# Kernel tuning notes

Measured on AMD Instinct MI355X. Metric: run time of the kernel, lower is better.

The kernel has to match this reference:

```python
import jax, jax.numpy as jnp
import numpy as np

EPS = 1e-08


def setup_inputs() -> dict:
    key = jax.random.key(0)
    k1, k2, k3 = jax.random.split(key, 3)
    B, T, IN, OUT = 32, 500, 2048, 1024
    x = jax.random.normal(k1, (B, T, IN), dtype=jnp.float32)
    # torch init: normal(mean=0, std=w_init_std*sqrt(1/input_shape))
    w = jax.random.normal(k2, (IN, OUT), dtype=jnp.float32) * np.sqrt(1.0 / IN)
    # b ~ N(1.0, 0.01), clamped >= 0
    b = jnp.clip(1.0 + 0.01 * jax.random.normal(k3, (OUT,), dtype=jnp.float32), 0.0, None)
    decay_m = jnp.array([0.6], dtype=jnp.float32)  # N(0.6, .01) clamped to [0,1]
    decay_s = jnp.array([0.9], dtype=jnp.float32)  # N(0.9, .01) clamped to [0,1]
    return {"x": x, "w": w, "b": b, "decay_m": decay_m, "decay_s": decay_s}


def reference(x, w, b, decay_m, decay_s):
    # x: [B, T, IN]; w: [IN, OUT]
    B, T, _ = x.shape
    OUT = w.shape[1]
    h = jnp.einsum('btc,cd->btd', x, w)          # [B, T, OUT]
    norm = jnp.sum(w * w, axis=0)                 # [OUT]
    dm = decay_m[0]
    ds = decay_s[0]
    inv_norm = 1.0 / (norm + EPS)
    zeros = jnp.zeros((B, OUT), dtype=x.dtype)
    # spk is never assigned a spike value in the original forward (spike_fn
    # is never applied), so it remains zero throughout.
    spk = zeros

    def step(carry, inp):
        M, S, E = carry
        E = dm * norm * (E + spk)                 # spk == 0 (faithful to source)
        M = dm * (M + inp)
        S = ds * (S + inp)
        mem = M - S - E
        mthr = mem * inv_norm - b                 # [B, OUT]
        return (M, S, E), mthr

    (_, _, _), spk_rec_t = jax.lax.scan(step, (zeros, zeros, zeros),
                                        jnp.swapaxes(h, 0, 1))  # [T, B, OUT]
    spk_rec = jnp.swapaxes(spk_rec_t, 0, 1)       # [B, T, OUT]
    loss = 0.5 * jnp.mean(spk_rec ** 2)
    return (spk_rec, loss)
```

## Files before the change

kernel.cpp:

```cpp
#include <hip/hip_runtime.h>


typedef __bf16 bf16x8 __attribute__((ext_vector_type(8)));
typedef __bf16 bf16x4 __attribute__((ext_vector_type(4)));
typedef float  f32x4  __attribute__((ext_vector_type(4)));

#define BDIM 32
#define TDIM 500
#define INDIM 2048
#define OUTDIM 1024
#define MROWS 16000
#define NCHUNK 25
#define CHLEN 20
#define OUT_ELEMS 16384000

__device__ __forceinline__ void gld_lds16(const void* g, void* l) {
    __builtin_amdgcn_global_load_lds(
        (const __attribute__((address_space(1))) unsigned int*)g,
        (__attribute__((address_space(3))) unsigned int*)l, 16, 0, 0);
}

__global__ void convert_x(const float* __restrict__ x, __bf16* __restrict__ xb) {
    size_t i = ((size_t)blockIdx.x * 256 + threadIdx.x) * 8;
    float4 a = *(const float4*)(x + i);
    float4 b = *(const float4*)(x + i + 4);
    bf16x8 o;
    o[0] = (__bf16)a.x; o[1] = (__bf16)a.y; o[2] = (__bf16)a.z; o[3] = (__bf16)a.w;
    o[4] = (__bf16)b.x; o[5] = (__bf16)b.y; o[6] = (__bf16)b.z; o[7] = (__bf16)b.w;
    *(bf16x8*)(xb + i) = o;
}

__global__ void transpose_w(const float* __restrict__ w, __bf16* __restrict__ wbt,
                            float* __restrict__ normAcc) {
    __shared__ float tile[32][33];
    __shared__ float red[8][33];
    const int tx = threadIdx.x;
    const int ty = threadIdx.y;
    const int d0 = blockIdx.x * 32;
    const int c0 = blockIdx.y * 32;
    float s = 0.f;
#pragma unroll
    for (int i = 0; i < 4; ++i) {
        int c = c0 + ty + i * 8;
        float v = w[(size_t)c * OUTDIM + d0 + tx];
        tile[ty + i * 8][tx] = v;
        s += v * v;
    }
    red[ty][tx] = s;
    __syncthreads();
#pragma unroll
    for (int i = 0; i < 4; ++i) {
        int d = d0 + ty + i * 8;
        wbt[(size_t)d * INDIM + c0 + tx] = (__bf16)tile[tx][ty + i * 8];
    }
    if (ty == 0) {
        float t = red[0][tx] + red[1][tx] + red[2][tx] + red[3][tx]
                + red[4][tx] + red[5][tx] + red[6][tx] + red[7][tx];
        atomicAdd(&normAcc[d0 + tx], t);
    }
}

__global__ __launch_bounds__(512, 2) void gemm_bf16(
    const __bf16* __restrict__ A,
    const __bf16* __restrict__ Bt,
    __bf16* __restrict__ H)
{
    constexpr int K  = INDIM;
    constexpr int NT = K / 32;
    __shared__ __align__(16) __bf16 As[4][256 * 32];
    __shared__ __align__(16) __bf16 Bs[4][256 * 32];

    const int tid  = threadIdx.x;
    const int wave = tid >> 6;
    const int lane = tid & 63;
    const int wm   = wave >> 2;
    const int wn   = wave & 3;

    const int orig = blockIdx.x;
    const int xcd = orig & 7, within = orig >> 3;
    const int wgid = (xcd < 4) ? (xcd * 32 + within)
                               : (128 + (xcd - 4) * 31 + within);
    const int bm = (wgid >> 2) * 256;
    const int bn = (wgid & 3) * 256;

    const int srow = lane >> 2;
    const int sseg = lane & 3;
    const int scol = (sseg ^ ((srow >> 1) & 3)) * 8;
    const int lds0 = (wave * 16) * 32;
    const int lds1 = (128 + wave * 16) * 32;
    int rA0 = bm +       wave * 16 + srow; if (rA0 > MROWS - 1) rA0 = MROWS - 1;
    int rA1 = bm + 128 + wave * 16 + srow; if (rA1 > MROWS - 1) rA1 = MROWS - 1;
    const __bf16* gA0 = A  + (size_t)rA0 * K + scol;
    const __bf16* gA1 = A  + (size_t)rA1 * K + scol;
    const __bf16* gB0 = Bt + (size_t)(bn +       wave * 16 + srow) * K + scol;
    const __bf16* gB1 = Bt + (size_t)(bn + 128 + wave * 16 + srow) * K + scol;

    const int mrow = lane & 15, quad = lane >> 4;
    const int swzq = quad ^ ((mrow >> 1) & 3);
    const int rdA = (wm * 128 + mrow) * 32 + swzq * 8;
    const int rdB = (wn * 64  + mrow) * 32 + swzq * 8;

    f32x4 acc[8][4] = {};

#define STAGE(tt) do { const int _b = (tt) & 3; const size_t _k = (size_t)(tt) * 32; \
        gld_lds16(gA0 + _k, &As[_b][lds0]);                                          \
        gld_lds16(gA1 + _k, &As[_b][lds1]);                                          \
        gld_lds16(gB0 + _k, &Bs[_b][lds0]);                                          \
        gld_lds16(gB1 + _k, &Bs[_b][lds1]); } while (0)

    STAGE(0); STAGE(1); STAGE(2); STAGE(3);
    asm volatile("s_waitcnt vmcnt(12)" ::: "memory");
    asm volatile("s_barrier" ::: "memory");

#pragma unroll 1
    for (int t = 0; t < NT; ++t) {
        const __bf16* as = As[t & 3];
        const __bf16* bs = Bs[t & 3];
        bf16x8 af[8], bfr[4];
#pragma unroll
        for (int i = 0; i < 8; ++i) af[i]  = *(const bf16x8*)&as[rdA + i * 512];
#pragma unroll
        for (int j = 0; j < 4; ++j) bfr[j] = *(const bf16x8*)&bs[rdB + j * 512];
#pragma unroll
        for (int i = 0; i < 8; ++i)
#pragma unroll
            for (int j = 0; j < 4; ++j)
                acc[i][j] = __builtin_amdgcn_mfma_f32_16x16x32_bf16(
                    af[i], bfr[j], acc[i][j], 0, 0, 0);
        asm volatile("s_barrier" ::: "memory");
        if (t + 4 < NT) STAGE(t + 4);
        if (t < NT - 4)       asm volatile("s_waitcnt vmcnt(12)" ::: "memory");
        else if (t == NT - 4) asm volatile("s_waitcnt vmcnt(8)"  ::: "memory");
        else if (t == NT - 3) asm volatile("s_waitcnt vmcnt(4)"  ::: "memory");
        else if (t == NT - 2) asm volatile("s_waitcnt vmcnt(0)"  ::: "memory");
        if (t < NT - 1) asm volatile("s_barrier" ::: "memory");
    }
#undef STAGE

    const int Rb = bm + wm * 128 + quad * 4;
    const int Cb = bn + wn * 64 + mrow;
#pragma unroll
    for (int i = 0; i < 8; ++i)
#pragma unroll
        for (int j = 0; j < 4; ++j)
#pragma unroll
            for (int r = 0; r < 4; ++r) {
                const int R = Rb + i * 16 + r;
                if (R < MROWS)
                    H[(size_t)R * OUTDIM + Cb + j * 16] = (__bf16)acc[i][j][r];
            }
}

__global__ void scan1(const __bf16* __restrict__ H,
                      f32x4* __restrict__ cM, f32x4* __restrict__ cS,
                      const float* __restrict__ dmp, const float* __restrict__ dsp) {
    const float dm = *dmp, ds = *dsp;
    const int c = blockIdx.x, b = blockIdx.y, tid = threadIdx.x;
    f32x4 M = {}, S = {};
    const __bf16* p = H + ((size_t)b * TDIM + c * CHLEN) * OUTDIM + tid * 4;
#pragma unroll 4
    for (int t = 0; t < CHLEN; ++t) {
        bf16x4 hv = *(const bf16x4*)(p + (size_t)t * OUTDIM);
        f32x4 h; h[0] = hv[0]; h[1] = hv[1]; h[2] = hv[2]; h[3] = hv[3];
        M = dm * (M + h);
        S = ds * (S + h);
    }
    const size_t idx = ((size_t)c * BDIM + b) * 256 + tid;
    cM[idx] = M;
    cS[idx] = S;
}

__global__ void scan2(float* __restrict__ cM, float* __restrict__ cS,
                      const float* __restrict__ dmp, const float* __restrict__ dsp) {
    const float dm = *dmp, ds = *dsp;
    float km = 1.f, ks = 1.f;
#pragma unroll
    for (int i = 0; i < CHLEN; ++i) { km *= dm; ks *= ds; }
    const int gid = blockIdx.x * 256 + threadIdx.x;
    const int b = gid >> 10, d = gid & 1023;
    float tM = 0.f, tS = 0.f;
    for (int c = 0; c < NCHUNK; ++c) {
        const size_t idx = (((size_t)c * BDIM + b) << 10) + d;
        float oM = cM[idx], oS = cS[idx];
        cM[idx] = tM; cS[idx] = tS;
        tM = km * tM + oM;
        tS = ks * tS + oS;
    }
}

__global__ void scan3(const __bf16* __restrict__ H,
                      const f32x4* __restrict__ cM, const f32x4* __restrict__ cS,
                      const float* __restrict__ normAcc, const float* __restrict__ bias,
                      const float* __restrict__ dmp, const float* __restrict__ dsp,
                      float* __restrict__ out, float* __restrict__ lossAcc,
                      unsigned* __restrict__ ticket) {
    const float dm = *dmp, ds = *dsp;
    const int c = blockIdx.x, b = blockIdx.y, tid = threadIdx.x;
    const size_t cidx = ((size_t)c * BDIM + b) * 256 + tid;
    f32x4 M = cM[cidx];
    f32x4 S = cS[cidx];
    f32x4 nv = *(const f32x4*)(normAcc + tid * 4);
    f32x4 inv;
    inv[0] = 1.f / (nv[0] + 1e-8f); inv[1] = 1.f / (nv[1] + 1e-8f);
    inv[2] = 1.f / (nv[2] + 1e-8f); inv[3] = 1.f / (nv[3] + 1e-8f);
    f32x4 bv = *(const f32x4*)(bias + tid * 4);

    const size_t rowbase = ((size_t)b * TDIM + c * CHLEN) * OUTDIM + tid * 4;
    const __bf16* p = H + rowbase;
    float* o = out + rowbase;
    float loss = 0.f;
#pragma unroll 4
    for (int t = 0; t < CHLEN; ++t) {
        bf16x4 hv = *(const bf16x4*)(p + (size_t)t * OUTDIM);
        f32x4 h; h[0] = hv[0]; h[1] = hv[1]; h[2] = hv[2]; h[3] = hv[3];
        M = dm * (M + h);
        S = ds * (S + h);
        f32x4 r = (M - S) * inv - bv;
        *(f32x4*)(o + (size_t)t * OUTDIM) = r;
        loss += r[0] * r[0] + r[1] * r[1] + r[2] * r[2] + r[3] * r[3];
    }
    __shared__ float red[256];
    red[tid] = loss;
    __syncthreads();
    for (int s = 128; s > 0; s >>= 1) {
        if (tid < s) red[tid] += red[tid + s];
        __syncthreads();
    }
    if (tid == 0) {
        atomicAdd(lossAcc, red[0]);
        __threadfence();
        unsigned t = atomicAdd(ticket, 1u);
        if (t == NCHUNK * BDIM - 1) {
            float total = atomicAdd(lossAcc, 0.0f);
            out[OUT_ELEMS] = 0.5f * total / (float)OUT_ELEMS;
        }
    }
}

#define OFF_H      ((size_t)0)
#define OFF_WBT    ((size_t)32768000)
#define OFF_NORM   ((size_t)36962304)
#define OFF_LOSS   ((size_t)36966400)
#define OFF_TICKET ((size_t)36966404)
#define OFF_CM     ((size_t)36966656)
#define OFF_CS     ((size_t)40243456)

extern "C" void kernel_launch(void* const* d_in, const int* in_sizes, int n_in,
                              void* d_out, int out_size, void* d_ws, size_t ws_size,
                              hipStream_t stream) {
    const float* x  = (const float*)d_in[0];
    const float* w  = (const float*)d_in[1];
    const float* bb = (const float*)d_in[2];
    const float* dm = (const float*)d_in[3];
    const float* ds = (const float*)d_in[4];

    char* ws = (char*)d_ws;
    __bf16*   H    = (__bf16*)(ws + OFF_H);
    __bf16*   WBT  = (__bf16*)(ws + OFF_WBT);
    float*    NORM = (float*)(ws + OFF_NORM);
    float*    LOSS = (float*)(ws + OFF_LOSS);
    unsigned* TICK = (unsigned*)(ws + OFF_TICKET);
    f32x4*    CM   = (f32x4*)(ws + OFF_CM);
    f32x4*    CS   = (f32x4*)(ws + OFF_CS);
    __bf16*   XB   = (__bf16*)d_out;
    float*    out  = (float*)d_out;

    hipMemsetAsync(ws + OFF_NORM, 0, 4096 + 256, stream);

    convert_x<<<16000, 256, 0, stream>>>(x, XB);
    transpose_w<<<dim3(32, 64), dim3(32, 8), 0, stream>>>(w, WBT, NORM);
    gemm_bf16<<<252, 512, 0, stream>>>(XB, WBT, H);
    scan1<<<dim3(NCHUNK, BDIM), 256, 0, stream>>>(H, CM, CS, dm, ds);
    scan2<<<128, 256, 0, stream>>>((float*)CM, (float*)CS, dm, ds);
    scan3<<<dim3(NCHUNK, BDIM), 256, 0, stream>>>(H, CM, CS, NORM, bb, dm, ds,
                                                  out, LOSS, TICK);
}
```

Measured before the change: 347.3 us.

## Fuse fp32-to-bf16 conversion of x into GEMM A-tile loading

Drops the separate convert_x kernel. The GEMM now reads fp32 x directly through register prefetch two steps ahead, converts it to bf16, and writes it into swizzled LDS, while B stays on direct global-to-LDS loads. The k-step is split into two half-tiles of 4x4 MFMAs with finer-grained waits and barriers. This removes a full write and re-read of the bf16 copy of x. In exchange the GEMM reads twice as many A bytes, holds more registers, and runs conversion ALU work inside the main loop.

```diff
diff --git a/kernel.cpp b/kernel.cpp
--- a/kernel.cpp
+++ b/kernel.cpp
@@ -18,16 +18,6 @@
     __builtin_amdgcn_global_load_lds(
         (const __attribute__((address_space(1))) unsigned int*)g,
         (__attribute__((address_space(3))) unsigned int*)l, 16, 0, 0);
-}
-
-__global__ void convert_x(const float* __restrict__ x, __bf16* __restrict__ xb) {
-    size_t i = ((size_t)blockIdx.x * 256 + threadIdx.x) * 8;
-    float4 a = *(const float4*)(x + i);
-    float4 b = *(const float4*)(x + i + 4);
-    bf16x8 o;
-    o[0] = (__bf16)a.x; o[1] = (__bf16)a.y; o[2] = (__bf16)a.z; o[3] = (__bf16)a.w;
-    o[4] = (__bf16)b.x; o[5] = (__bf16)b.y; o[6] = (__bf16)b.z; o[7] = (__bf16)b.w;
-    *(bf16x8*)(xb + i) = o;
 }
 
 __global__ void transpose_w(const float* __restrict__ w, __bf16* __restrict__ wbt,
@@ -60,8 +50,8 @@
     }
 }
 
-__global__ __launch_bounds__(512, 2) void gemm_bf16(
-    const __bf16* __restrict__ A,
+__global__ __launch_bounds__(512, 2) void gemm_fused(
+    const float* __restrict__ A,
     const __bf16* __restrict__ Bt,
     __bf16* __restrict__ H)
 {
@@ -83,17 +73,21 @@
     const int bm = (wgid >> 2) * 256;
     const int bn = (wgid & 3) * 256;
 
+    const int rloc = tid >> 1;
+    const int asub = tid & 1;
+    int arow = bm + rloc; if (arow > MROWS - 1) arow = MROWS - 1;
+    const float* aSrc = A + (size_t)arow * K + asub * 16;
+    const int fA = (rloc >> 1) & 3;
+    const int wbOff0 = rloc * 32 + ((2 * asub)     ^ fA) * 8;
+    const int wbOff1 = rloc * 32 + ((2 * asub + 1) ^ fA) * 8;
+
     const int srow = lane >> 2;
     const int sseg = lane & 3;
     const int scol = (sseg ^ ((srow >> 1) & 3)) * 8;
-    const int lds0 = (wave * 16) * 32;
-    const int lds1 = (128 + wave * 16) * 32;
-    int rA0 = bm +       wave * 16 + srow; if (rA0 > MROWS - 1) rA0 = MROWS - 1;
-    int rA1 = bm + 128 + wave * 16 + srow; if (rA1 > MROWS - 1) rA1 = MROWS - 1;
-    const __bf16* gA0 = A  + (size_t)rA0 * K + scol;
-    const __bf16* gA1 = A  + (size_t)rA1 * K + scol;
-    const __bf16* gB0 = Bt + (size_t)(bn +       wave * 16 + srow) * K + scol;
-    const __bf16* gB1 = Bt + (size_t)(bn + 128 + wave * 16 + srow) * K + scol;
+    const __bf16* gB0 = Bt + (size_t)(bn + (wave * 2 + 0) * 16 + srow) * K + scol;
+    const __bf16* gB1 = Bt + (size_t)(bn + (wave * 2 + 1) * 16 + srow) * K + scol;
+    const int ldsB0 = (wave * 2 + 0) * 512;
+    const int ldsB1 = (wave * 2 + 1) * 512;
 
     const int mrow = lane & 15, quad = lane >> 4;
     const int swzq = quad ^ ((mrow >> 1) & 3);
@@ -101,41 +95,85 @@
     const int rdB = (wn * 64  + mrow) * 32 + swzq * 8;
 
     f32x4 acc[8][4] = {};
-
-#define STAGE(tt) do { const int _b = (tt) & 3; const size_t _k = (size_t)(tt) * 32; \
-        gld_lds16(gA0 + _k, &As[_b][lds0]);                                          \
-        gld_lds16(gA1 + _k, &As[_b][lds1]);                                          \
-        gld_lds16(gB0 + _k, &Bs[_b][lds0]);                                          \
-        gld_lds16(gB1 + _k, &Bs[_b][lds1]); } while (0)
-
-    STAGE(0); STAGE(1); STAGE(2); STAGE(3);
-    asm volatile("s_waitcnt vmcnt(12)" ::: "memory");
+    f32x4 gl0[4], gl1[4];
+
+#define ALOAD(G, TT) do { const float* s_ = aSrc + (size_t)(TT) * 32;           \
+        G[0] = *(const f32x4*)(s_);      G[1] = *(const f32x4*)(s_ + 4);        \
+        G[2] = *(const f32x4*)(s_ + 8);  G[3] = *(const f32x4*)(s_ + 12); } while (0)
+
+#define AWB(G, TT) do { __bf16* ad_ = &As[(TT) & 3][0]; bf16x8 o0_, o1_;        \
+        o0_[0]=(__bf16)G[0][0]; o0_[1]=(__bf16)G[0][1]; o0_[2]=(__bf16)G[0][2]; \
+        o0_[3]=(__bf16)G[0][3]; o0_[4]=(__bf16)G[1][0]; o0_[5]=(__bf16)G[1][1]; \
+        o0_[6]=(__bf16)G[1][2]; o0_[7]=(__bf16)G[1][3];                         \
+        o1_[0]=(__bf16)G[2][0]; o1_[1]=(__bf16)G[2][1]; o1_[2]=(__bf16)G[2][2]; \
+        o1_[3]=(__bf16)G[2][3]; o1_[4]=(__bf16)G[3][0]; o1_[5]=(__bf16)G[3][1]; \
+        o1_[6]=(__bf16)G[3][2]; o1_[7]=(__bf16)G[3][3];                         \
+        *(bf16x8*)(ad_ + wbOff0) = o0_; *(bf16x8*)(ad_ + wbOff1) = o1_; } while (0)
+
+#define BSTAGE(TT) do {                                                          \
+        gld_lds16(gB0 + (size_t)(TT) * 32, &Bs[(TT) & 3][ldsB0]);                \
+        gld_lds16(gB1 + (size_t)(TT) * 32, &Bs[(TT) & 3][ldsB1]); } while (0)
+
+    ALOAD(gl0, 0);
+    ALOAD(gl1, 1);
+    asm volatile("s_waitcnt vmcnt(4)" ::: "memory");
+    AWB(gl0, 0);
+    ALOAD(gl0, 2);
+    asm volatile("s_waitcnt vmcnt(4)" ::: "memory");
+    AWB(gl1, 1);
+    ALOAD(gl1, 3);
+    asm volatile("s_waitcnt vmcnt(4)" ::: "memory");
+    AWB(gl0, 2);
+    BSTAGE(0); BSTAGE(1); BSTAGE(2);
+    asm volatile("s_waitcnt vmcnt(4) lgkmcnt(0)" ::: "memory");
     asm volatile("s_barrier" ::: "memory");
 
+#define KSTEP(T, GI, GC) do {                                                    \
+        const __bf16* as_ = &As[(T) & 3][0];                                     \
+        const __bf16* bs_ = &Bs[(T) & 3][0];                                     \
+                        \
+        if ((T) + 4 < NT) ALOAD(GI, (T) + 4);                                    \
+        if ((T) <= NT - 5)      asm volatile("s_waitcnt vmcnt(6)" ::: "memory"); \
+        else if ((T) <= NT - 3) asm volatile("s_waitcnt vmcnt(2)" ::: "memory"); \
+        else if ((T) == NT - 2) asm volatile("s_waitcnt vmcnt(0)" ::: "memory"); \
+        if ((T) + 3 < NT) AWB(GC, (T) + 3);                                      \
+        bf16x8 a_[4], b_[4];                                                     \
+        _Pragma("unroll")                                                        \
+        for (int i = 0; i < 4; ++i) a_[i] = *(const bf16x8*)&as_[rdA + i * 512]; \
+        _Pragma("unroll")                                                        \
+        for (int j = 0; j < 4; ++j) b_[j] = *(const bf16x8*)&bs_[rdB + j * 512]; \
+        asm volatile("s_waitcnt lgkmcnt(0)" ::: "memory");                       \
+        _Pragma("unroll")                                                        \
+        for (int i = 0; i < 4; ++i)                                              \
+        _Pragma("unroll")                                                        \
+            for (int j = 0; j < 4; ++j)                                          \
+                acc[i][j] = __builtin_amdgcn_mfma_f32_16x16x32_bf16(             \
+                    a_[i], b_[j], acc[i][j], 0, 0, 0);                           \
+        asm volatile("s_barrier" ::: "memory");                                  \
+                                     \
+        if ((T) + 3 < NT) BSTAGE((T) + 3);                                       \
+        _Pragma("unroll")                                                        \
+        for (int i = 0; i < 4; ++i)                                              \
+            a_[i] = *(const bf16x8*)&as_[rdA + 2048 + i * 512];                  \
+        asm volatile("s_waitcnt lgkmcnt(0)" ::: "memory");                       \
+        _Pragma("unroll")                                                        \
+        for (int i = 0; i < 4; ++i)                                              \
+        _Pragma("unroll")                                                        \
+            for (int j = 0; j < 4; ++j)                                          \
+                acc[4 + i][j] = __builtin_amdgcn_mfma_f32_16x16x32_bf16(         \
+                    a_[i], b_[j], acc[4 + i][j], 0, 0, 0);                       \
+        asm volatile("s_barrier" ::: "memory");                                  \
+    } while (0)
+
 #pragma unroll 1
-    for (int t = 0; t < NT; ++t) {
-        const __bf16* as = As[t & 3];
-        const __bf16* bs = Bs[t & 3];
-        bf16x8 af[8], bfr[4];
-#pragma unroll
-        for (int i = 0; i < 8; ++i) af[i]  = *(const bf16x8*)&as[rdA + i * 512];
-#pragma unroll
-        for (int j = 0; j < 4; ++j) bfr[j] = *(const bf16x8*)&bs[rdB + j * 512];
-#pragma unroll
-        for (int i = 0; i < 8; ++i)
-#pragma unroll
-            for (int j = 0; j < 4; ++j)
-                acc[i][j] = __builtin_amdgcn_mfma_f32_16x16x32_bf16(
-                    af[i], bfr[j], acc[i][j], 0, 0, 0);
-        asm volatile("s_barrier" ::: "memory");
-        if (t + 4 < NT) STAGE(t + 4);
-        if (t < NT - 4)       asm volatile("s_waitcnt vmcnt(12)" ::: "memory");
-        else if (t == NT - 4) asm volatile("s_waitcnt vmcnt(8)"  ::: "memory");
-        else if (t == NT - 3) asm volatile("s_waitcnt vmcnt(4)"  ::: "memory");
-        else if (t == NT - 2) asm volatile("s_waitcnt vmcnt(0)"  ::: "memory");
-        if (t < NT - 1) asm volatile("s_barrier" ::: "memory");
-    }
-#undef STAGE
+    for (int t = 0; t < NT; t += 2) {
+        KSTEP(t,     gl0, gl1);
+        KSTEP(t + 1, gl1, gl0);
+    }
+#undef KSTEP
+#undef ALOAD
+#undef AWB
+#undef BSTAGE
 
     const int Rb = bm + wm * 128 + quad * 4;
     const int Cb = bn + wn * 64 + mrow;
@@ -262,14 +300,12 @@
     unsigned* TICK = (unsigned*)(ws + OFF_TICKET);
     f32x4*    CM   = (f32x4*)(ws + OFF_CM);
     f32x4*    CS   = (f32x4*)(ws + OFF_CS);
-    __bf16*   XB   = (__bf16*)d_out;
     float*    out  = (float*)d_out;
 
     hipMemsetAsync(ws + OFF_NORM, 0, 4096 + 256, stream);
 
-    convert_x<<<16000, 256, 0, stream>>>(x, XB);
     transpose_w<<<dim3(32, 64), dim3(32, 8), 0, stream>>>(w, WBT, NORM);
-    gemm_bf16<<<252, 512, 0, stream>>>(XB, WBT, H);
+    gemm_fused<<<252, 512, 0, stream>>>(x, WBT, H);
     scan1<<<dim3(NCHUNK, BDIM), 256, 0, stream>>>(H, CM, CS, dm, ds);
     scan2<<<128, 256, 0, stream>>>((float*)CM, (float*)CS, dm, ds);
     scan3<<<dim3(NCHUNK, BDIM), 256, 0, stream>>>(H, CM, CS, NORM, bb, dm, ds,
```

New measurement: 343.4 us. Within noise of the previous version (-1.1%).

## Restructure GEMM mainloop into quadrant-split double-buffered K64 pipeline with interleaved loads

Applied to the files above, without the earlier changes.

Rewrites the bf16 GEMM main loop to use K-steps of 64 with a two-buffer LDS scheme. Each 256x256 tile is split into quadrants (A halves × B halves), and global→LDS loads for the next tile are interleaved between the four MFMA quadrant phases, each phase guarded by its own barrier. It also raises MFMA wave priority around compute blocks, with the aim of hiding load latency and cutting LDS read pressure per MFMA. The cost is more barriers per iteration and a more fragile, hand-tuned vmcnt schedule.

```diff
diff --git a/kernel.cpp b/kernel.cpp
--- a/kernel.cpp
+++ b/kernel.cpp
@@ -66,9 +66,9 @@
     __bf16* __restrict__ H)
 {
     constexpr int K  = INDIM;
-    constexpr int NT = K / 32;
-    __shared__ __align__(16) __bf16 As[4][256 * 32];
-    __shared__ __align__(16) __bf16 Bs[4][256 * 32];
+    constexpr int NT = K / 64;
+    __shared__ __align__(16) __bf16 SA[2][2][2][4096];
+    __shared__ __align__(16) __bf16 SB[2][2][2][4096];
 
     const int tid  = threadIdx.x;
     const int wave = tid >> 6;
@@ -86,69 +86,108 @@
     const int srow = lane >> 2;
     const int sseg = lane & 3;
     const int scol = (sseg ^ ((srow >> 1) & 3)) * 8;
-    const int lds0 = (wave * 16) * 32;
-    const int lds1 = (128 + wave * 16) * 32;
-    int rA0 = bm +       wave * 16 + srow; if (rA0 > MROWS - 1) rA0 = MROWS - 1;
-    int rA1 = bm + 128 + wave * 16 + srow; if (rA1 > MROWS - 1) rA1 = MROWS - 1;
-    const __bf16* gA0 = A  + (size_t)rA0 * K + scol;
-    const __bf16* gA1 = A  + (size_t)rA1 * K + scol;
-    const __bf16* gB0 = Bt + (size_t)(bn +       wave * 16 + srow) * K + scol;
-    const __bf16* gB1 = Bt + (size_t)(bn + 128 + wave * 16 + srow) * K + scol;
+    int ra0 = bm +       wave * 16 + srow; if (ra0 > MROWS - 1) ra0 = MROWS - 1;
+    int ra1 = bm + 128 + wave * 16 + srow; if (ra1 > MROWS - 1) ra1 = MROWS - 1;
+    const __bf16* pA0 = A  + (size_t)ra0 * K + scol;
+    const __bf16* pA1 = A  + (size_t)ra1 * K + scol;
+    const __bf16* pB0 = Bt + (size_t)(bn +       wave * 16 + srow) * K + scol;
+    const __bf16* pB1 = Bt + (size_t)(bn + 128 + wave * 16 + srow) * K + scol;
+    const int sdst = wave * 512;
 
     const int mrow = lane & 15, quad = lane >> 4;
     const int swzq = quad ^ ((mrow >> 1) & 3);
-    const int rdA = (wm * 128 + mrow) * 32 + swzq * 8;
-    const int rdB = (wn * 64  + mrow) * 32 + swzq * 8;
+    const int rdA = (wm * 64 + mrow) * 32 + swzq * 8;
+    const int rdB = (wn * 32 + mrow) * 32 + swzq * 8;
 
     f32x4 acc[8][4] = {};
-
-#define STAGE(tt) do { const int _b = (tt) & 3; const size_t _k = (size_t)(tt) * 32; \
-        gld_lds16(gA0 + _k, &As[_b][lds0]);                                          \
-        gld_lds16(gA1 + _k, &As[_b][lds1]);                                          \
-        gld_lds16(gB0 + _k, &Bs[_b][lds0]);                                          \
-        gld_lds16(gB1 + _k, &Bs[_b][lds1]); } while (0)
-
-    STAGE(0); STAGE(1); STAGE(2); STAGE(3);
-    asm volatile("s_waitcnt vmcnt(12)" ::: "memory");
+    bf16x8 a[4][2], b[2][2];
+
+#define STG_A(NB, HH, T1) do { const __bf16* p_ = (HH) ? pA1 : pA0;            \
+        gld_lds16(p_ + (size_t)(T1) * 64,      &SA[NB][HH][0][sdst]);          \
+        gld_lds16(p_ + (size_t)(T1) * 64 + 32, &SA[NB][HH][1][sdst]); } while (0)
+#define STG_B(NB, HH, T1) do { const __bf16* p_ = (HH) ? pB1 : pB0;            \
+        gld_lds16(p_ + (size_t)(T1) * 64,      &SB[NB][HH][0][sdst]);          \
+        gld_lds16(p_ + (size_t)(T1) * 64 + 32, &SB[NB][HH][1][sdst]); } while (0)
+#define RD_A(BUF, HH) do { _Pragma("unroll")                                   \
+        for (int i = 0; i < 4; ++i) {                                          \
+            a[i][0] = *(const bf16x8*)&SA[BUF][HH][0][rdA + i * 512];          \
+            a[i][1] = *(const bf16x8*)&SA[BUF][HH][1][rdA + i * 512]; } } while (0)
+#define RD_B(BUF, HH) do { _Pragma("unroll")                                   \
+        for (int j = 0; j < 2; ++j) {                                          \
+            b[j][0] = *(const bf16x8*)&SB[BUF][HH][0][rdB + j * 512];          \
+            b[j][1] = *(const bf16x8*)&SB[BUF][HH][1][rdB + j * 512]; } } while (0)
+#define MM(HM, HN) do { __builtin_amdgcn_s_setprio(1);                         \
+        _Pragma("unroll")                                                      \
+        for (int i = 0; i < 4; ++i)                                            \
+        _Pragma("unroll")                                                      \
+        for (int j = 0; j < 2; ++j) {                                          \
+            acc[(HM)*4+i][(HN)*2+j] = __builtin_amdgcn_mfma_f32_16x16x32_bf16( \
+                a[i][0], b[j][0], acc[(HM)*4+i][(HN)*2+j], 0, 0, 0);           \
+            acc[(HM)*4+i][(HN)*2+j] = __builtin_amdgcn_mfma_f32_16x16x32_bf16( \
+                a[i][1], b[j][1], acc[(HM)*4+i][(HN)*2+j], 0, 0, 0); }         \
+        __builtin_amdgcn_s_setprio(0); } while (0)
+
+#define TILE(T, CUR, NB) do {                                                  \
+        const bool st_   = (T) + 1 < NT;                                       \
+        const bool last_ = (T) == NT - 1;                                      \
+                                                           \
+        RD_A(CUR, 0); RD_B(CUR, 0);                                            \
+        if (st_) STG_A(NB, 0, (T) + 1);                                        \
+        if (!last_) asm volatile("s_waitcnt vmcnt(4)" ::: "memory");           \
+        else        asm volatile("s_waitcnt vmcnt(2)" ::: "memory");           \
+        asm volatile("s_barrier" ::: "memory");                                \
+        MM(0, 0);                                                              \
+                                                  \
+        RD_B(CUR, 1);                                                          \
+        if (st_) STG_B(NB, 0, (T) + 1);                                        \
+        if (!last_) asm volatile("s_waitcnt vmcnt(4)" ::: "memory");           \
+        else        asm volatile("s_waitcnt vmcnt(0)" ::: "memory");           \
+        asm volatile("s_barrier" ::: "memory");                                \
+        MM(0, 1);                                                              \
+                                                  \
+        RD_A(CUR, 1);                                                          \
+        if (st_) STG_B(NB, 1, (T) + 1);                                        \
+        asm volatile("s_barrier" ::: "memory");                                \
+        MM(1, 1);                                                              \
+                                              \
+        RD_B(CUR, 0);                                                          \
+        if (st_) STG_A(NB, 1, (T) + 1);                                        \
+        if (st_) asm volatile("s_waitcnt vmcnt(4)" ::: "memory");              \
+        asm volatile("s_barrier" ::: "memory");                                \
+        MM(1, 0);                                                              \
+    } while (0)
+
+    STG_A(0, 0, 0); STG_B(0, 0, 0); STG_B(0, 1, 0); STG_A(0, 1, 0);
+    asm volatile("s_waitcnt vmcnt(4)" ::: "memory");
     asm volatile("s_barrier" ::: "memory");
 
 #pragma unroll 1
-    for (int t = 0; t < NT; ++t) {
-        const __bf16* as = As[t & 3];
-        const __bf16* bs = Bs[t & 3];
-        bf16x8 af[8], bfr[4];
-#pragma unroll
-        for (int i = 0; i < 8; ++i) af[i]  = *(const bf16x8*)&as[rdA + i * 512];
-#pragma unroll
-        for (int j = 0; j < 4; ++j) bfr[j] = *(const bf16x8*)&bs[rdB + j * 512];
-#pragma unroll
-        for (int i = 0; i < 8; ++i)
-#pragma unroll
-            for (int j = 0; j < 4; ++j)
-                acc[i][j] = __builtin_amdgcn_mfma_f32_16x16x32_bf16(
-                    af[i], bfr[j], acc[i][j], 0, 0, 0);
-        asm volatile("s_barrier" ::: "memory");
-        if (t + 4 < NT) STAGE(t + 4);
-        if (t < NT - 4)       asm volatile("s_waitcnt vmcnt(12)" ::: "memory");
-        else if (t == NT - 4) asm volatile("s_waitcnt vmcnt(8)"  ::: "memory");
-        else if (t == NT - 3) asm volatile("s_waitcnt vmcnt(4)"  ::: "memory");
-        else if (t == NT - 2) asm volatile("s_waitcnt vmcnt(0)"  ::: "memory");
-        if (t < NT - 1) asm volatile("s_barrier" ::: "memory");
-    }
-#undef STAGE
-
-    const int Rb = bm + wm * 128 + quad * 4;
-    const int Cb = bn + wn * 64 + mrow;
-#pragma unroll
-    for (int i = 0; i < 8; ++i)
-#pragma unroll
-        for (int j = 0; j < 4; ++j)
-#pragma unroll
-            for (int r = 0; r < 4; ++r) {
-                const int R = Rb + i * 16 + r;
-                if (R < MROWS)
-                    H[(size_t)R * OUTDIM + Cb + j * 16] = (__bf16)acc[i][j][r];
-            }
+    for (int tt = 0; tt < NT; tt += 2) {
+        TILE(tt,     0, 1);
+        TILE(tt + 1, 1, 0);
+    }
+#undef TILE
+#undef MM
+#undef RD_B
+#undef RD_A
+#undef STG_B
+#undef STG_A
+
+#pragma unroll
+    for (int hm = 0; hm < 2; ++hm)
+#pragma unroll
+        for (int i = 0; i < 4; ++i)
+#pragma unroll
+            for (int hn = 0; hn < 2; ++hn)
+#pragma unroll
+                for (int j = 0; j < 2; ++j)
+#pragma unroll
+                    for (int r = 0; r < 4; ++r) {
+                        const int R = bm + hm * 128 + wm * 64 + i * 16 + quad * 4 + r;
+                        const int C = bn + hn * 128 + wn * 32 + j * 16 + mrow;
+                        if (R < MROWS)
+                            H[(size_t)R * OUTDIM + C] = (__bf16)acc[hm * 4 + i][hn * 2 + j][r];
+                    }
 }
 
 __global__ void scan1(const __bf16* __restrict__ H,
```

Measured after the change: 333.8 us. 1.04x faster.
